# Performance work log

Hardware: AMD Instinct MI355X
Metric: run time of the kernel (lower is better)

## Reference

```python
import jax, jax.numpy as jnp
import numpy as np

B, N, M, D, OUT, K = 8, 32, 64, 128, 128, 3
EPS = 1e-5


def batchnorm(x, g, b):
    # training-mode BatchNorm2d over NCHW (stats over B,H,W per channel, biased var)
    mean = x.mean((0, 2, 3), keepdims=True)
    var = ((x - mean) ** 2).mean((0, 2, 3), keepdims=True)
    return g[None, :, None, None] * (x - mean) * jax.lax.rsqrt(var + EPS) + b[None, :, None, None]


def mycorr(x):
    # Pearson correlation between nodes along feature dim: x (B,M,N,D) -> (B,M,N,N)
    xc = x - x.mean(-1, keepdims=True)
    num = jnp.einsum('bmid,bmjd->bmij', xc, xc)
    nrm = jnp.sqrt((xc * xc).sum(-1))
    return num / (nrm[:, :, :, None] * nrm[:, :, None, :] + 1e-8)


def attention(x, W_fc1, W_fc2):
    # x: (B,M,N,D). AdaptiveAvgPool2d((None,1)) over the concat [Wh_i, pos*Wh_j]
    # equals 0.5*(mean_d Wh_i + mean_d(pos*Wh_j)); pos=1 where Wh_i==Wh_j else 2.
    adj = mycorr(x)
    mean_i = x.mean(-1)                       # (B,M,N)
    xi = x[:, :, :, None, :]                  # (B,M,N,1,D)
    xj = x[:, :, None, :, :]                  # (B,M,1,N,D)
    alt_mean = jnp.where(xi == xj, xj, 2.0 * xj).mean(-1)  # (B,M,N,N)
    e = 0.5 * (mean_i[:, :, :, None] + alt_mean)            # (B,M,N,N)
    ef = e.reshape(e.shape[0], e.shape[1], -1)              # (B,M,N*N) pair channels
    h = jax.nn.relu(jnp.einsum('rp,bmp->bmr', W_fc1, ef))
    e2 = jax.nn.sigmoid(jnp.einsum('pr,bmr->bmp', W_fc2, h)).reshape(e.shape)
    att = jax.nn.softmax(jnp.where(adj > 0, e2, jnp.float32(-1e12)), axis=-1)
    return jnp.einsum('bmij,bmjd->bmid', att, x)


def setup_inputs() -> dict:
    key = jax.random.key(0)
    ks = jax.random.split(key, 8)
    P, r, s = N * N, (N * N) // 2, 0.05
    return {
        'x': jax.random.normal(ks[0], (B, N, M, D), jnp.float32),
        'W_sc': jax.random.normal(ks[1], (OUT, M), jnp.float32) * s,
        'g_sc': jnp.ones(OUT, jnp.float32), 'b_sc': jnp.zeros(OUT, jnp.float32),
        'W_l1': jax.random.normal(ks[2], (M, M), jnp.float32) * s,
        'g1': jnp.ones(M, jnp.float32), 'b1': jnp.zeros(M, jnp.float32),
        'W_fc1': jax.random.normal(ks[3], (r, P), jnp.float32) * s,
        'W_fc2': jax.random.normal(ks[4], (P, r), jnp.float32) * s,
        'g2': jnp.ones(M, jnp.float32), 'b2': jnp.zeros(M, jnp.float32),
        'W_dw': jax.random.normal(ks[5], (N, 1, K, K), jnp.float32) * s,
        'g3': jnp.ones(N, jnp.float32), 'b3': jnp.zeros(N, jnp.float32),
        'W_l3': jax.random.normal(ks[6], (OUT, M), jnp.float32) * s,
    }


def reference(x, W_sc, g_sc, b_sc, W_l1, g1, b1, W_fc1, W_fc2, g2, b2, W_dw, g3, b3, W_l3):
    xm = jnp.transpose(x, (0, 2, 1, 3))  # (B,M,N,D)
    # shortcut: 1x1 conv over head channel + BN (stride=1 path)
    shortcut = batchnorm(jnp.einsum('om,bmnd->bond', W_sc, xm), g_sc, b_sc)
    # layer_1: 1x1 conv, BN, global node attention, BN, ReLU
    out = batchnorm(jnp.einsum('cm,bmnd->bcnd', W_l1, xm), g1, b1)
    out = attention(out, W_fc1, W_fc2)
    out = jax.nn.relu(batchnorm(out, g2, b2))
    # layer_2: depthwise KxK conv over (head, dim) per node, BN, ReLU
    out = jnp.transpose(out, (0, 2, 1, 3))  # (B,N,M,D)
    pad = K // 2
    out = jax.lax.conv_general_dilated(out, W_dw, (1, 1), ((pad, pad), (pad, pad)),
                                       feature_group_count=N,
                                       dimension_numbers=('NCHW', 'OIHW', 'NCHW'))
    out = jax.nn.relu(batchnorm(out, g3, b3))
    # layer_3: 1x1 conv to out_channels heads + residual
    out = jnp.transpose(out, (0, 2, 1, 3))  # (B,M,N,D)
    out = jnp.einsum('om,bmnd->bond', W_l3, out) + shortcut
    return jnp.transpose(out, (0, 2, 1, 3))  # (B,N,OUT,D)
```

## Files before the change

### kernel.cpp

```cpp
#include <hip/hip_runtime.h>
#include <math.h>

#define EPS 1e-5f


__device__ __forceinline__ void fma4(float4& a, float s, const float4& v) {
    a.x += s * v.x; a.y += s * v.y; a.z += s * v.z; a.w += s * v.w;
}

__global__ __launch_bounds__(256) void k0_prep(
    const float* __restrict__ Wsc, const float* __restrict__ Wl1,
    const float* __restrict__ Wl3, float* __restrict__ Wt,
    float* __restrict__ Wt3, float* __restrict__ stats)
{
    int idx = blockIdx.x * 256 + threadIdx.x;
    if (idx < 12288) {
        int m = idx / 192, cc = idx % 192;
        Wt[idx] = (cc < 128) ? Wsc[(size_t)cc * 64 + m]
                             : Wl1[(size_t)(cc - 128) * 64 + m];
    } else if (idx < 20480) {
        int k = idx - 12288;
        int m = k >> 7, o = k & 127;
        Wt3[k] = Wl3[(size_t)o * 64 + m];
    } else if (idx < 21504) {
        stats[idx - 20480] = 0.f;
    }
}

__global__ __launch_bounds__(256, 3) void k1_matmul_stats(
    const float* __restrict__ x, const float* __restrict__ Wt,
    const float* __restrict__ Wfc1, float* __restrict__ t_sc,
    float* __restrict__ t_l1, float* __restrict__ C1,
    float* __restrict__ stats)
{
    int g  = blockIdx.x;
    int bn = blockIdx.y;
    __shared__ __align__(16) float s_x[64 * 144];
    __shared__ __align__(16) float s_w[64 * 64];
    int t = threadIdx.x;

    if (g == 3) {
#pragma unroll
        for (int rr = 0; rr < 2; rr++) {
            int r = bn * 2 + rr;
            *(float4*)(s_x + t * 4) =
                *(const float4*)(Wfc1 + (size_t)r * 1024 + t * 4);
            __syncthreads();
            if (t < 32) {
                float rs = 0.f, cs = 0.f;
#pragma unroll
                for (int j = 0; j < 32; j++) {
                    rs += s_x[t * 32 + j];
                    cs += s_x[j * 32 + t];
                }
                C1[r * 32 + t] = (rs + 2.f * cs - s_x[t * 33]) * (1.0f / 256.0f);
            }
            __syncthreads();
        }
        return;
    }

    int b = bn >> 5, n = bn & 31;
    const float4* xg = (const float4*)(x + (size_t)bn * 8192);
    for (int i = t; i < 2048; i += 256) {
        int row = i >> 5, j = i & 31;
        *(float4*)(s_x + row * 144 + j * 4 + ((j >> 3) << 2)) = xg[i];
    }
    for (int i = t; i < 1024; i += 256) {
        int m = i >> 4, ch = (i & 15) * 4;
        *(float4*)(s_w + i * 4) =
            *(const float4*)(Wt + (size_t)m * 192 + g * 64 + ch);
    }
    __syncthreads();

    int wv = t >> 6, lane = t & 63;
    int dl = lane & 15, g4 = lane >> 4;
    int d0 = dl * 8;
    int c0 = wv * 16 + g4 * 4;
    int xoff = d0 + ((dl >> 2) << 2);

    float4 acc[4][2];
#pragma unroll
    for (int i = 0; i < 4; i++) { acc[i][0] = make_float4(0,0,0,0); acc[i][1] = make_float4(0,0,0,0); }

#pragma unroll 4
    for (int m = 0; m < 64; m += 2) {
        const float* xr = s_x + m * 144 + xoff;
        float4 x00 = *(const float4*)(xr);
        float4 x01 = *(const float4*)(xr + 4);
        float4 x10 = *(const float4*)(xr + 144);
        float4 x11 = *(const float4*)(xr + 148);
        float4 w0 = *(const float4*)(s_w + m * 64 + c0);
        float4 w1 = *(const float4*)(s_w + (m + 1) * 64 + c0);
        fma4(acc[0][0], w0.x, x00); fma4(acc[0][1], w0.x, x01);
        fma4(acc[1][0], w0.y, x00); fma4(acc[1][1], w0.y, x01);
        fma4(acc[2][0], w0.z, x00); fma4(acc[2][1], w0.z, x01);
        fma4(acc[3][0], w0.w, x00); fma4(acc[3][1], w0.w, x01);
        fma4(acc[0][0], w1.x, x10); fma4(acc[0][1], w1.x, x11);
        fma4(acc[1][0], w1.y, x10); fma4(acc[1][1], w1.y, x11);
        fma4(acc[2][0], w1.z, x10); fma4(acc[2][1], w1.z, x11);
        fma4(acc[3][0], w1.w, x10); fma4(acc[3][1], w1.w, x11);
    }

#pragma unroll
    for (int i = 0; i < 4; i++) {
        int cc = g * 64 + c0 + i;
        float4 v0 = acc[i][0], v1 = acc[i][1];
        float* dst;
        if (cc < 128) dst = t_sc + (((size_t)bn * 128 + cc)) * 128 + d0;
        else          dst = t_l1 + (((size_t)(b * 64 + (cc - 128))) * 32 + n) * 128 + d0;
        *(float4*)dst = v0;
        *(float4*)(dst + 4) = v1;
        float s = v0.x + v0.y + v0.z + v0.w + v1.x + v1.y + v1.z + v1.w;
        float q = v0.x*v0.x + v0.y*v0.y + v0.z*v0.z + v0.w*v0.w
                + v1.x*v1.x + v1.y*v1.y + v1.z*v1.z + v1.w*v1.w;
#pragma unroll
        for (int off = 8; off > 0; off >>= 1) {
            s += __shfl_down(s, off, 16);
            q += __shfl_down(q, off, 16);
        }
        if (dl == 0) {
            if (cc < 128) {
                atomicAdd(&stats[cc], s);
                atomicAdd(&stats[cc + 128], q);
            } else {
                atomicAdd(&stats[256 + (cc - 128)], s);
                atomicAdd(&stats[320 + (cc - 128)], q);
            }
        }
    }
}

__device__ __forceinline__ int yb(int r) { return r * 132 + ((r >> 2) << 3); }

__global__ __launch_bounds__(256) void k2_attn_prep(
    const float* __restrict__ t_l1, const float* __restrict__ g1,
    const float* __restrict__ b1, const float* __restrict__ stats,
    const float* __restrict__ Wfc1, const float* __restrict__ C1,
    float* __restrict__ y_g, float* __restrict__ H,
    unsigned int* __restrict__ maskbits)
{
    int bm = blockIdx.x;
    int t  = threadIdx.x;
    __shared__ __align__(16) float y_s[4288];
    __shared__ float S_s[32];
    __shared__ unsigned int m_s[32];
    __shared__ int anom_cnt;
    __shared__ int anom_p[64];
    __shared__ float anom_v[64];
    int m = bm & 63;
    float mean = stats[256 + m] * (1.0f / 32768.0f);
    float var  = stats[320 + m] * (1.0f / 32768.0f) - mean * mean;
    float a = g1[m] * rsqrtf(var + EPS);
    float c = b1[m] - a * mean;

    if (t == 0) anom_cnt = 0;
    if (t < 32) m_s[t] = 0u;
    const float4* src = (const float4*)(t_l1 + (size_t)bm * 4096);
    for (int i = t; i < 1024; i += 256) {
        float4 v = src[i];
        v.x = a * v.x + c; v.y = a * v.y + c; v.z = a * v.z + c; v.w = a * v.w + c;
        int row = i >> 5, col = (i & 31) * 4;
        *(float4*)(y_s + yb(row) + col) = v;
    }
    __syncthreads();

    {
        int r = t >> 3, j = t & 7;
        float s = 0.f;
        const float* yr = y_s + yb(r) + j * 16;
#pragma unroll
        for (int dd = 0; dd < 16; dd++) s += yr[dd];
#pragma unroll
        for (int off = 4; off > 0; off >>= 1) s += __shfl_down(s, off, 8);
        if (j == 0) S_s[r] = s;
    }
    __syncthreads();

    int i = t >> 3, j0 = (t & 7) * 4;
    float dot[4] = {0.f, 0.f, 0.f, 0.f};
    float eqs[4] = {0.f, 0.f, 0.f, 0.f};
    const float* yi = y_s + yb(i);
    const float* yj[4] = { y_s + yb(j0), y_s + yb(j0 + 1),
                           y_s + yb(j0 + 2), y_s + yb(j0 + 3) };
    for (int dq = 0; dq < 32; dq++) {
        float4 a4 = *(const float4*)(yi + dq * 4);
#pragma unroll
        for (int q = 0; q < 4; q++) {
            float4 b4 = *(const float4*)(yj[q] + dq * 4);
            dot[q] += a4.x * b4.x + a4.y * b4.y + a4.z * b4.z + a4.w * b4.w;
            eqs[q] += (a4.x == b4.x ? b4.x : 0.f) + (a4.y == b4.y ? b4.y : 0.f)
                    + (a4.z == b4.z ? b4.z : 0.f) + (a4.w == b4.w ? b4.w : 0.f);
        }
    }
    float Si = S_s[i];
    unsigned int bits = 0u;
#pragma unroll
    for (int q = 0; q < 4; q++) {
        int j = j0 + q;
        float Sj = S_s[j];
        float num = dot[q] - Si * Sj * (1.0f / 128.0f);
        if (num > 0.f) bits |= (1u << j);
        if (j != i && eqs[q] != 0.f) {
            int idx = atomicAdd(&anom_cnt, 1);
            if (idx < 64) {
                anom_p[idx] = i * 32 + j;
                anom_v[idx] = eqs[q] * (1.0f / 256.0f);
            }
        }
    }
    atomicOr(&m_s[i], bits);
    __syncthreads();
    if (t < 32) maskbits[bm * 32 + t] = m_s[t];

    int cnt = anom_cnt; if (cnt > 64) cnt = 64;
#pragma unroll
    for (int rr = 0; rr < 2; rr++) {
        int r = t * 2 + rr;
        const float4* c1r = (const float4*)(C1 + r * 32);
        float acc = 0.f;
#pragma unroll
        for (int kk = 0; kk < 8; kk++) {
            float4 cv = c1r[kk];
            acc += cv.x * S_s[kk * 4 + 0] + cv.y * S_s[kk * 4 + 1]
                 + cv.z * S_s[kk * 4 + 2] + cv.w * S_s[kk * 4 + 3];
        }
        for (int a2 = 0; a2 < cnt; a2++)
            acc -= Wfc1[(size_t)r * 1024 + anom_p[a2]] * anom_v[a2];
        H[(size_t)bm * 512 + r] = fmaxf(acc, 0.f);
    }

    float4* yd = (float4*)(y_g + (size_t)bm * 4096);
    for (int idx = t; idx < 1024; idx += 256) {
        int row = idx >> 5, col = (idx & 31) * 4;
        yd[idx] = *(const float4*)(y_s + yb(row) + col);
    }
}

template<int KDIM, int MODE>
__global__ __launch_bounds__(256) void k3_gemm(
    const float* __restrict__ A, const float* __restrict__ Bm,
    float* __restrict__ C, int NC)
{
    __shared__ __align__(16) float lds[4 * 2304];
    int t = threadIdx.x;
    int w = t >> 6, l = t & 63;
    int ct = blockIdx.x, rt = blockIdx.y;
    int row0 = rt * 32, col0 = ct * 32;
    float* As = lds + w * 2304;
    float* Bs = As + 1152;
    int rg = l >> 3;
    int cg = l & 7;
    int kq = (l & 7) * 4;
    constexpr int SLABS = KDIM / 128;

    float4 acc[4];
#pragma unroll
    for (int ii = 0; ii < 4; ii++) acc[ii] = make_float4(0,0,0,0);

    float4 av[4], bv[4], av2[4], bv2[4];
    int k0 = w * 32;
#pragma unroll
    for (int rr = 0; rr < 4; rr++) {
        int r = rg + rr * 8;
        av[rr] = *(const float4*)(A  + (size_t)(row0 + r) * KDIM + k0 + kq);
        bv[rr] = *(const float4*)(Bm + (size_t)(col0 + r) * KDIM + k0 + kq);
    }

    for (int s = 0; s < SLABS; s++) {
#pragma unroll
        for (int rr = 0; rr < 4; rr++) {
            int r = rg + rr * 8;
            As[(kq + 0) * 36 + r] = av[rr].x; As[(kq + 1) * 36 + r] = av[rr].y;
            As[(kq + 2) * 36 + r] = av[rr].z; As[(kq + 3) * 36 + r] = av[rr].w;
            Bs[(kq + 0) * 36 + r] = bv[rr].x; Bs[(kq + 1) * 36 + r] = bv[rr].y;
            Bs[(kq + 2) * 36 + r] = bv[rr].z; Bs[(kq + 3) * 36 + r] = bv[rr].w;
        }
        if (s + 1 < SLABS) {
            int kn = (4 * (s + 1) + w) * 32;
#pragma unroll
            for (int rr = 0; rr < 4; rr++) {
                int r = rg + rr * 8;
                av2[rr] = *(const float4*)(A  + (size_t)(row0 + r) * KDIM + kn + kq);
                bv2[rr] = *(const float4*)(Bm + (size_t)(col0 + r) * KDIM + kn + kq);
            }
        }
#pragma unroll
        for (int k = 0; k < 32; k++) {
            float4 a = *(const float4*)(As + k * 36 + rg * 4);
            float4 b = *(const float4*)(Bs + k * 36 + cg * 4);
            fma4(acc[0], a.x, b);
            fma4(acc[1], a.y, b);
            fma4(acc[2], a.z, b);
            fma4(acc[3], a.w, b);
        }
#pragma unroll
        for (int rr = 0; rr < 4; rr++) { av[rr] = av2[rr]; bv[rr] = bv2[rr]; }
    }

    __syncthreads();
    float* red = lds;
#pragma unroll
    for (int ii = 0; ii < 4; ii++)
        *(float4*)(red + w * 1024 + (rg * 4 + ii) * 32 + cg * 4) = acc[ii];
    __syncthreads();

    int r = t >> 3, c4 = (t & 7) * 4;
    float4 s0 = *(const float4*)(red + r * 32 + c4);
    float4 s1 = *(const float4*)(red + 1024 + r * 32 + c4);
    float4 s2 = *(const float4*)(red + 2048 + r * 32 + c4);
    float4 s3 = *(const float4*)(red + 3072 + r * 32 + c4);
    float4 v;
    v.x = s0.x + s1.x + s2.x + s3.x;
    v.y = s0.y + s1.y + s2.y + s3.y;
    v.z = s0.z + s1.z + s2.z + s3.z;
    v.w = s0.w + s1.w + s2.w + s3.w;
    if (MODE == 0) {
        v.x = fmaxf(v.x, 0.f); v.y = fmaxf(v.y, 0.f);
        v.z = fmaxf(v.z, 0.f); v.w = fmaxf(v.w, 0.f);
    } else {
        v.x = 1.0f / (1.0f + expf(-v.x)); v.y = 1.0f / (1.0f + expf(-v.y));
        v.z = 1.0f / (1.0f + expf(-v.z)); v.w = 1.0f / (1.0f + expf(-v.w));
    }
    *(float4*)(C + (size_t)(row0 + r) * NC + col0 + c4) = v;
}

__global__ __launch_bounds__(256) void k4_attn_apply(
    const float* __restrict__ E2, const unsigned int* __restrict__ maskbits,
    const float* __restrict__ y_g, float* __restrict__ att_out,
    float* __restrict__ stats)
{
    int bm = blockIdx.x;
    int t  = threadIdx.x;
    __shared__ __align__(16) float att_s[32 * 33];
    __shared__ __align__(16) float y_sh[32 * 128];
    __shared__ float redS[4], redQ[4];

    const float4* ysrc = (const float4*)(y_g + (size_t)bm * 4096);
    float4* yds = (float4*)y_sh;
    for (int i = t; i < 1024; i += 256) yds[i] = ysrc[i];

    {
        int r = t >> 3, j0 = (t & 7) * 4;
        unsigned int mk = maskbits[bm * 32 + r];
        float4 e4 = *(const float4*)(E2 + (size_t)bm * 1024 + r * 32 + j0);
        float v0 = ((mk >> (j0 + 0)) & 1u) ? e4.x : -1e12f;
        float v1 = ((mk >> (j0 + 1)) & 1u) ? e4.y : -1e12f;
        float v2 = ((mk >> (j0 + 2)) & 1u) ? e4.z : -1e12f;
        float v3 = ((mk >> (j0 + 3)) & 1u) ? e4.w : -1e12f;
        float mx = fmaxf(fmaxf(v0, v1), fmaxf(v2, v3));
#pragma unroll
        for (int off = 1; off < 8; off <<= 1) mx = fmaxf(mx, __shfl_xor(mx, off, 8));
        float e0 = __expf(v0 - mx), e1 = __expf(v1 - mx);
        float e2 = __expf(v2 - mx), e3 = __expf(v3 - mx);
        float s = e0 + e1 + e2 + e3;
#pragma unroll
        for (int off = 1; off < 8; off <<= 1) s += __shfl_xor(s, off, 8);
        float inv = 1.0f / s;
        att_s[r * 33 + j0 + 0] = e0 * inv;
        att_s[r * 33 + j0 + 1] = e1 * inv;
        att_s[r * 33 + j0 + 2] = e2 * inv;
        att_s[r * 33 + j0 + 3] = e3 * inv;
    }
    __syncthreads();

    int tx = t & 31, ty = t >> 5;
    int dq = tx * 4;
    int i0 = ty * 4;
    float4 acc0 = make_float4(0,0,0,0), acc1 = make_float4(0,0,0,0);
    float4 acc2 = make_float4(0,0,0,0), acc3 = make_float4(0,0,0,0);
    for (int j = 0; j < 32; j++) {
        float4 yv = *(const float4*)(y_sh + j * 128 + dq);
        float w0 = att_s[(i0 + 0) * 33 + j];
        float w1 = att_s[(i0 + 1) * 33 + j];
        float w2 = att_s[(i0 + 2) * 33 + j];
        float w3 = att_s[(i0 + 3) * 33 + j];
        fma4(acc0, w0, yv);
        fma4(acc1, w1, yv);
        fma4(acc2, w2, yv);
        fma4(acc3, w3, yv);
    }
    float ssum = 0.f, sq = 0.f;
    float4 accs[4] = {acc0, acc1, acc2, acc3};
#pragma unroll
    for (int ii = 0; ii < 4; ii++) {
        float4 acc = accs[ii];
        *(float4*)(att_out + (size_t)bm * 4096 + (i0 + ii) * 128 + dq) = acc;
        ssum += acc.x + acc.y + acc.z + acc.w;
        sq   += acc.x * acc.x + acc.y * acc.y + acc.z * acc.z + acc.w * acc.w;
    }
#pragma unroll
    for (int off = 32; off > 0; off >>= 1) {
        ssum += __shfl_down(ssum, off, 64);
        sq   += __shfl_down(sq, off, 64);
    }
    int wave = t >> 6, lane = t & 63;
    if (lane == 0) { redS[wave] = ssum; redQ[wave] = sq; }
    __syncthreads();
    if (t == 0) {
        float S = redS[0] + redS[1] + redS[2] + redS[3];
        float Q = redQ[0] + redQ[1] + redQ[2] + redQ[3];
        int m = bm & 63;
        atomicAdd(&stats[384 + m], S);
        atomicAdd(&stats[448 + m], Q);
    }
}

__global__ __launch_bounds__(256) void k5_conv(
    const float* __restrict__ att_out, const float* __restrict__ Wdw,
    const float* __restrict__ g2, const float* __restrict__ b2,
    float* __restrict__ stats, float* __restrict__ v_g)
{
    int bn = blockIdx.x;
    int b = bn >> 5, n = bn & 31;
    int t = threadIdx.x;
    __shared__ __align__(16) float z_s[66 * 130];
    __shared__ float a2_s[64], c2_s[64];
    __shared__ float redS[4], redQ[4];

    if (t < 64) {
        float mean = stats[384 + t] * (1.0f / 32768.0f);
        float var  = stats[448 + t] * (1.0f / 32768.0f) - mean * mean;
        float a = g2[t] * rsqrtf(var + EPS);
        a2_s[t] = a; c2_s[t] = b2[t] - a * mean;
    }
    for (int i = t; i < 66 * 130; i += 256) z_s[i] = 0.f;
    __syncthreads();

    for (int i = t; i < 2048; i += 256) {
        int m = i >> 5, c4 = (i & 31) * 4;
        float4 vv = *(const float4*)(att_out + (((size_t)(b * 64 + m)) * 32 + n) * 128 + c4);
        float a = a2_s[m], c = c2_s[m];
        float* dst = z_s + (m + 1) * 130 + c4 + 1;
        dst[0] = fmaxf(a * vv.x + c, 0.f);
        dst[1] = fmaxf(a * vv.y + c, 0.f);
        dst[2] = fmaxf(a * vv.z + c, 0.f);
        dst[3] = fmaxf(a * vv.w + c, 0.f);
    }
    float w[9];
#pragma unroll
    for (int i = 0; i < 9; i++) w[i] = Wdw[n * 9 + i];
    __syncthreads();

    int tx = t & 31, ty = t >> 5;
    int d0 = tx * 4;
    float ssum = 0.f, sq = 0.f;
#pragma unroll
    for (int rr = 0; rr < 8; rr++) {
        int h = ty * 8 + rr;
        float o0 = 0.f, o1 = 0.f, o2 = 0.f, o3 = 0.f;
#pragma unroll
        for (int dh = 0; dh < 3; dh++) {
            const float* zr = z_s + (h + dh) * 130 + d0;
#pragma unroll
            for (int dw = 0; dw < 3; dw++) {
                float wv = w[dh * 3 + dw];
                o0 += wv * zr[dw + 0];
                o1 += wv * zr[dw + 1];
                o2 += wv * zr[dw + 2];
                o3 += wv * zr[dw + 3];
            }
        }
        *(float4*)(v_g + ((size_t)bn * 64 + h) * 128 + d0) = make_float4(o0, o1, o2, o3);
        ssum += o0 + o1 + o2 + o3;
        sq   += o0 * o0 + o1 * o1 + o2 * o2 + o3 * o3;
    }
#pragma unroll
    for (int off = 32; off > 0; off >>= 1) {
        ssum += __shfl_down(ssum, off, 64);
        sq   += __shfl_down(sq, off, 64);
    }
    int wave = t >> 6, lane = t & 63;
    if (lane == 0) { redS[wave] = ssum; redQ[wave] = sq; }
    __syncthreads();
    if (t == 0) {
        atomicAdd(&stats[512 + n], redS[0] + redS[1] + redS[2] + redS[3]);
        atomicAdd(&stats[544 + n], redQ[0] + redQ[1] + redQ[2] + redQ[3]);
    }
}

__global__ __launch_bounds__(256, 3) void k6_final(
    const float* __restrict__ v_g, const float* __restrict__ t_sc,
    const float* __restrict__ Wt3, const float* __restrict__ g3,
    const float* __restrict__ b3, const float* __restrict__ gsc,
    const float* __restrict__ bsc, const float* __restrict__ stats,
    float* __restrict__ outp)
{
    int oh = blockIdx.x;
    int bn = blockIdx.y;
    int b = bn >> 5, n = bn & 31;
    int t = threadIdx.x;
    __shared__ __align__(16) float z_s[64 * 144];
    __shared__ __align__(16) float s_w[64 * 64];

    float mean3 = stats[512 + n] * (1.0f / 65536.0f);
    float var3  = stats[544 + n] * (1.0f / 65536.0f) - mean3 * mean3;
    float a3 = g3[n] * rsqrtf(var3 + EPS);
    float c3 = b3[n] - a3 * mean3;

    const float4* vsrc = (const float4*)(v_g + (size_t)bn * 8192);
    for (int i = t; i < 2048; i += 256) {
        float4 vv = vsrc[i];
        float4 r;
        r.x = fmaxf(a3 * vv.x + c3, 0.f);
        r.y = fmaxf(a3 * vv.y + c3, 0.f);
        r.z = fmaxf(a3 * vv.z + c3, 0.f);
        r.w = fmaxf(a3 * vv.w + c3, 0.f);
        int row = i >> 5, j = i & 31;
        *(float4*)(z_s + row * 144 + j * 4 + ((j >> 3) << 2)) = r;
    }
    for (int i = t; i < 1024; i += 256) {
        int m = i >> 4, ch = (i & 15) * 4;
        *(float4*)(s_w + i * 4) =
            *(const float4*)(Wt3 + (size_t)m * 128 + oh * 64 + ch);
    }
    __syncthreads();

    int wv = t >> 6, lane = t & 63;
    int dl = lane & 15, g4 = lane >> 4;
    int d0 = dl * 8;
    int c0 = wv * 16 + g4 * 4;
    int xoff = d0 + ((dl >> 2) << 2);

    float4 acc[4][2];
#pragma unroll
    for (int i = 0; i < 4; i++) { acc[i][0] = make_float4(0,0,0,0); acc[i][1] = make_float4(0,0,0,0); }

#pragma unroll 4
    for (int m = 0; m < 64; m += 2) {
        const float* xr = z_s + m * 144 + xoff;
        float4 x00 = *(const float4*)(xr);
        float4 x01 = *(const float4*)(xr + 4);
        float4 x10 = *(const float4*)(xr + 144);
        float4 x11 = *(const float4*)(xr + 148);
        float4 w0 = *(const float4*)(s_w + m * 64 + c0);
        float4 w1 = *(const float4*)(s_w + (m + 1) * 64 + c0);
        fma4(acc[0][0], w0.x, x00); fma4(acc[0][1], w0.x, x01);
        fma4(acc[1][0], w0.y, x00); fma4(acc[1][1], w0.y, x01);
        fma4(acc[2][0], w0.z, x00); fma4(acc[2][1], w0.z, x01);
        fma4(acc[3][0], w0.w, x00); fma4(acc[3][1], w0.w, x01);
        fma4(acc[0][0], w1.x, x10); fma4(acc[0][1], w1.x, x11);
        fma4(acc[1][0], w1.y, x10); fma4(acc[1][1], w1.y, x11);
        fma4(acc[2][0], w1.z, x10); fma4(acc[2][1], w1.z, x11);
        fma4(acc[3][0], w1.w, x10); fma4(acc[3][1], w1.w, x11);
    }

#pragma unroll
    for (int i = 0; i < 4; i++) {
        int o = oh * 64 + c0 + i;
        float msc = stats[o] * (1.0f / 32768.0f);
        float vsc = stats[128 + o] * (1.0f / 32768.0f) - msc * msc;
        float asc = gsc[o] * rsqrtf(vsc + EPS);
        float csc = bsc[o] - asc * msc;
        const float* ts = t_sc + ((size_t)bn * 128 + o) * 128 + d0;
        float4 t0 = *(const float4*)(ts);
        float4 t1 = *(const float4*)(ts + 4);
        float4 o0 = acc[i][0], o1 = acc[i][1];
        o0.x += asc * t0.x + csc; o0.y += asc * t0.y + csc;
        o0.z += asc * t0.z + csc; o0.w += asc * t0.w + csc;
        o1.x += asc * t1.x + csc; o1.y += asc * t1.y + csc;
        o1.z += asc * t1.z + csc; o1.w += asc * t1.w + csc;
        float* dst = outp + (((size_t)(b * 32 + n)) * 128 + o) * 128 + d0;
        *(float4*)dst = o0;
        *(float4*)(dst + 4) = o1;
    }
}

extern "C" void kernel_launch(void* const* d_in, const int* in_sizes, int n_in,
                              void* d_out, int out_size, void* d_ws, size_t ws_size,
                              hipStream_t stream)
{
    const float* x    = (const float*)d_in[0];
    const float* Wsc  = (const float*)d_in[1];
    const float* gsc  = (const float*)d_in[2];
    const float* bsc  = (const float*)d_in[3];
    const float* Wl1  = (const float*)d_in[4];
    const float* g1   = (const float*)d_in[5];
    const float* b1   = (const float*)d_in[6];
    const float* Wfc1 = (const float*)d_in[7];
    const float* Wfc2 = (const float*)d_in[8];
    const float* g2   = (const float*)d_in[9];
    const float* b2   = (const float*)d_in[10];
    const float* Wdw  = (const float*)d_in[11];
    const float* g3   = (const float*)d_in[12];
    const float* b3   = (const float*)d_in[13];
    const float* Wl3  = (const float*)d_in[14];
    float* outp = (float*)d_out;

    float* ws = (float*)d_ws;
    float* stats = ws;
    float* t_sc  = ws + 1024;
    float* t_l1  = t_sc + 4194304;
    float* y_g   = t_l1 + 2097152;
    float* C1    = y_g + 2097152;
    float* H     = C1 + 16384;
    float* E2    = H + 262144;
    unsigned int* maskb = (unsigned int*)(E2 + 524288);
    float* Wt    = (float*)(maskb + 16384);
    float* Wt3   = Wt + 12288;

    k0_prep<<<84, 256, 0, stream>>>(Wsc, Wl1, Wl3, Wt, Wt3, stats);
    k1_matmul_stats<<<dim3(4, 256), 256, 0, stream>>>(x, Wt, Wfc1, t_sc, t_l1, C1, stats);
    k2_attn_prep<<<512, 256, 0, stream>>>(t_l1, g1, b1, stats, Wfc1, C1, y_g, H, maskb);
    k3_gemm<512, 1><<<dim3(32, 16), 256, 0, stream>>>(H, Wfc2, E2, 1024);
    k4_attn_apply<<<512, 256, 0, stream>>>(E2, maskb, y_g, t_l1, stats);
    k5_conv<<<256, 256, 0, stream>>>(t_l1, Wdw, g2, b2, stats, y_g);
    k6_final<<<dim3(2, 256), 256, 0, stream>>>(y_g, t_sc, Wt3, g3, b3, gsc, bsc, stats, outp);
}
```

Measured before the change: 196.1 us.

## Fuse pipeline stages into persistent megakernel with global grid barriers

Replaces the six stage kernels after prep with one persistent kernel of 512 blocks. The stages are separated by a software grid barrier built on atomics in workspace memory, and the Wfc1 row/column-sum precompute moves into the prep kernel. The aim is to remove per-launch overhead and tail gaps between the small stages. In exchange, every stage is tied to a fixed 512-block decomposition with two blocks per CU, and the barrier can deadlock if not all blocks are co-resident.

```diff
diff --git a/kernel.cpp b/kernel.cpp
--- a/kernel.cpp
+++ b/kernel.cpp
@@ -2,6 +2,7 @@
 #include <math.h>
 
 #define EPS 1e-5f
+#define NBLK 512
 
 
 __device__ __forceinline__ void fma4(float4& a, float s, const float4& v) {
@@ -10,559 +11,579 @@
 
 __global__ __launch_bounds__(256) void k0_prep(
     const float* __restrict__ Wsc, const float* __restrict__ Wl1,
-    const float* __restrict__ Wl3, float* __restrict__ Wt,
-    float* __restrict__ Wt3, float* __restrict__ stats)
+    const float* __restrict__ Wl3, const float* __restrict__ Wfc1,
+    float* __restrict__ Wt, float* __restrict__ Wt3,
+    float* __restrict__ stats, unsigned int* __restrict__ bar,
+    float* __restrict__ C1)
 {
-    int idx = blockIdx.x * 256 + threadIdx.x;
-    if (idx < 12288) {
-        int m = idx / 192, cc = idx % 192;
-        Wt[idx] = (cc < 128) ? Wsc[(size_t)cc * 64 + m]
-                             : Wl1[(size_t)(cc - 128) * 64 + m];
-    } else if (idx < 20480) {
-        int k = idx - 12288;
-        int m = k >> 7, o = k & 127;
-        Wt3[k] = Wl3[(size_t)o * 64 + m];
-    } else if (idx < 21504) {
-        stats[idx - 20480] = 0.f;
-    }
-}
-
-__global__ __launch_bounds__(256, 3) void k1_matmul_stats(
-    const float* __restrict__ x, const float* __restrict__ Wt,
-    const float* __restrict__ Wfc1, float* __restrict__ t_sc,
-    float* __restrict__ t_l1, float* __restrict__ C1,
-    float* __restrict__ stats)
-{
-    int g  = blockIdx.x;
-    int bn = blockIdx.y;
-    __shared__ __align__(16) float s_x[64 * 144];
-    __shared__ __align__(16) float s_w[64 * 64];
+    int bx = blockIdx.x;
     int t = threadIdx.x;
-
-    if (g == 3) {
+    if (bx < 84) {
+        int idx = bx * 256 + t;
+        if (idx < 12288) {
+            int m = idx / 192, cc = idx % 192;
+            Wt[idx] = (cc < 128) ? Wsc[(size_t)cc * 64 + m]
+                                 : Wl1[(size_t)(cc - 128) * 64 + m];
+        } else if (idx < 20480) {
+            int k = idx - 12288;
+            int m = k >> 7, o = k & 127;
+            Wt3[k] = Wl3[(size_t)o * 64 + m];
+        } else if (idx < 21504) {
+            stats[idx - 20480] = 0.f;
+        }
+        if (idx == 0) { bar[0] = 0u; bar[1] = 0u; }
+    } else {
+        __shared__ float s[1024];
 #pragma unroll
         for (int rr = 0; rr < 2; rr++) {
-            int r = bn * 2 + rr;
-            *(float4*)(s_x + t * 4) =
+            int r = (bx - 84) * 2 + rr;
+            *(float4*)(s + t * 4) =
                 *(const float4*)(Wfc1 + (size_t)r * 1024 + t * 4);
             __syncthreads();
             if (t < 32) {
                 float rs = 0.f, cs = 0.f;
 #pragma unroll
                 for (int j = 0; j < 32; j++) {
-                    rs += s_x[t * 32 + j];
-                    cs += s_x[j * 32 + t];
+                    rs += s[t * 32 + j];
+                    cs += s[j * 32 + t];
                 }
-                C1[r * 32 + t] = (rs + 2.f * cs - s_x[t * 33]) * (1.0f / 256.0f);
+                C1[r * 32 + t] = (rs + 2.f * cs - s[t * 33]) * (1.0f / 256.0f);
             }
             __syncthreads();
         }
-        return;
-    }
-
-    int b = bn >> 5, n = bn & 31;
-    const float4* xg = (const float4*)(x + (size_t)bn * 8192);
-    for (int i = t; i < 2048; i += 256) {
-        int row = i >> 5, j = i & 31;
-        *(float4*)(s_x + row * 144 + j * 4 + ((j >> 3) << 2)) = xg[i];
-    }
-    for (int i = t; i < 1024; i += 256) {
-        int m = i >> 4, ch = (i & 15) * 4;
-        *(float4*)(s_w + i * 4) =
-            *(const float4*)(Wt + (size_t)m * 192 + g * 64 + ch);
-    }
+    }
+}
+
+__device__ __forceinline__ void gsync(unsigned int* bar) {
     __syncthreads();
-
-    int wv = t >> 6, lane = t & 63;
-    int dl = lane & 15, g4 = lane >> 4;
-    int d0 = dl * 8;
-    int c0 = wv * 16 + g4 * 4;
-    int xoff = d0 + ((dl >> 2) << 2);
-
-    float4 acc[4][2];
-#pragma unroll
-    for (int i = 0; i < 4; i++) { acc[i][0] = make_float4(0,0,0,0); acc[i][1] = make_float4(0,0,0,0); }
-
+    if (threadIdx.x == 0) {
+        __threadfence();
+        unsigned int g = __hip_atomic_load(bar + 1, __ATOMIC_ACQUIRE,
+                                           __HIP_MEMORY_SCOPE_AGENT);
+        unsigned int a = __hip_atomic_fetch_add(bar, 1u, __ATOMIC_ACQ_REL,
+                                                __HIP_MEMORY_SCOPE_AGENT);
+        if (a == NBLK - 1u) {
+            __hip_atomic_store(bar, 0u, __ATOMIC_RELAXED,
+                               __HIP_MEMORY_SCOPE_AGENT);
+            __hip_atomic_fetch_add(bar + 1, 1u, __ATOMIC_ACQ_REL,
+                                   __HIP_MEMORY_SCOPE_AGENT);
+        } else {
+            while (__hip_atomic_load(bar + 1, __ATOMIC_ACQUIRE,
+                                     __HIP_MEMORY_SCOPE_AGENT) == g)
+                __builtin_amdgcn_s_sleep(8);
+        }
+        __threadfence();
+    }
+    __syncthreads();
+}
+
+__device__ __forceinline__ int yb(int r) { return r * 132 + ((r >> 2) << 3); }
+
+__global__ __launch_bounds__(256, 2) void mega(
+    const float* __restrict__ x, const float* __restrict__ Wt,
+    const float* __restrict__ Wt3, const float* __restrict__ Wfc1,
+    const float* __restrict__ Wfc2,
+    const float* __restrict__ g1, const float* __restrict__ b1,
+    const float* __restrict__ g2, const float* __restrict__ b2,
+    const float* __restrict__ g3, const float* __restrict__ b3,
+    const float* __restrict__ gsc, const float* __restrict__ bsc,
+    const float* __restrict__ Wdw,
+    float* __restrict__ t_sc, float* __restrict__ t_l1,
+    float* __restrict__ y_g, float* __restrict__ C1,
+    float* __restrict__ H, float* __restrict__ E2,
+    unsigned int* __restrict__ maskb, float* __restrict__ stats,
+    unsigned int* __restrict__ bar, float* __restrict__ outp)
+{
+    __shared__ __align__(16) float smem[13312];
+    int bid = blockIdx.x;
+    int t = threadIdx.x;
+
+    {
+        float* s_x = smem;
+        float* s_w = smem + 9216;
+        for (int u = bid; u < 768; u += NBLK) {
+            __syncthreads();
+            int g = u >> 8, bn = u & 255;
+            int b = bn >> 5, n = bn & 31;
+            const float4* xg = (const float4*)(x + (size_t)bn * 8192);
+            for (int i = t; i < 2048; i += 256) {
+                int row = i >> 5, j = i & 31;
+                *(float4*)(s_x + row * 144 + j * 4 + ((j >> 3) << 2)) = xg[i];
+            }
+            for (int i = t; i < 1024; i += 256) {
+                int m = i >> 4, ch = (i & 15) * 4;
+                *(float4*)(s_w + i * 4) =
+                    *(const float4*)(Wt + (size_t)m * 192 + g * 64 + ch);
+            }
+            __syncthreads();
+
+            int wv = t >> 6, lane = t & 63;
+            int dl = lane & 15, g4 = lane >> 4;
+            int d0 = dl * 8;
+            int c0 = wv * 16 + g4 * 4;
+            int xoff = d0 + ((dl >> 2) << 2);
+
+            float4 acc[4][2];
+#pragma unroll
+            for (int i = 0; i < 4; i++) {
+                acc[i][0] = make_float4(0,0,0,0);
+                acc[i][1] = make_float4(0,0,0,0);
+            }
 #pragma unroll 4
-    for (int m = 0; m < 64; m += 2) {
-        const float* xr = s_x + m * 144 + xoff;
-        float4 x00 = *(const float4*)(xr);
-        float4 x01 = *(const float4*)(xr + 4);
-        float4 x10 = *(const float4*)(xr + 144);
-        float4 x11 = *(const float4*)(xr + 148);
-        float4 w0 = *(const float4*)(s_w + m * 64 + c0);
-        float4 w1 = *(const float4*)(s_w + (m + 1) * 64 + c0);
-        fma4(acc[0][0], w0.x, x00); fma4(acc[0][1], w0.x, x01);
-        fma4(acc[1][0], w0.y, x00); fma4(acc[1][1], w0.y, x01);
-        fma4(acc[2][0], w0.z, x00); fma4(acc[2][1], w0.z, x01);
-        fma4(acc[3][0], w0.w, x00); fma4(acc[3][1], w0.w, x01);
-        fma4(acc[0][0], w1.x, x10); fma4(acc[0][1], w1.x, x11);
-        fma4(acc[1][0], w1.y, x10); fma4(acc[1][1], w1.y, x11);
-        fma4(acc[2][0], w1.z, x10); fma4(acc[2][1], w1.z, x11);
-        fma4(acc[3][0], w1.w, x10); fma4(acc[3][1], w1.w, x11);
-    }
-
-#pragma unroll
-    for (int i = 0; i < 4; i++) {
-        int cc = g * 64 + c0 + i;
-        float4 v0 = acc[i][0], v1 = acc[i][1];
-        float* dst;
-        if (cc < 128) dst = t_sc + (((size_t)bn * 128 + cc)) * 128 + d0;
-        else          dst = t_l1 + (((size_t)(b * 64 + (cc - 128))) * 32 + n) * 128 + d0;
-        *(float4*)dst = v0;
-        *(float4*)(dst + 4) = v1;
-        float s = v0.x + v0.y + v0.z + v0.w + v1.x + v1.y + v1.z + v1.w;
-        float q = v0.x*v0.x + v0.y*v0.y + v0.z*v0.z + v0.w*v0.w
-                + v1.x*v1.x + v1.y*v1.y + v1.z*v1.z + v1.w*v1.w;
-#pragma unroll
-        for (int off = 8; off > 0; off >>= 1) {
-            s += __shfl_down(s, off, 16);
-            q += __shfl_down(q, off, 16);
-        }
-        if (dl == 0) {
-            if (cc < 128) {
-                atomicAdd(&stats[cc], s);
-                atomicAdd(&stats[cc + 128], q);
-            } else {
-                atomicAdd(&stats[256 + (cc - 128)], s);
-                atomicAdd(&stats[320 + (cc - 128)], q);
-            }
-        }
-    }
-}
-
-__device__ __forceinline__ int yb(int r) { return r * 132 + ((r >> 2) << 3); }
-
-__global__ __launch_bounds__(256) void k2_attn_prep(
-    const float* __restrict__ t_l1, const float* __restrict__ g1,
-    const float* __restrict__ b1, const float* __restrict__ stats,
-    const float* __restrict__ Wfc1, const float* __restrict__ C1,
-    float* __restrict__ y_g, float* __restrict__ H,
-    unsigned int* __restrict__ maskbits)
-{
-    int bm = blockIdx.x;
-    int t  = threadIdx.x;
-    __shared__ __align__(16) float y_s[4288];
-    __shared__ float S_s[32];
-    __shared__ unsigned int m_s[32];
-    __shared__ int anom_cnt;
-    __shared__ int anom_p[64];
-    __shared__ float anom_v[64];
-    int m = bm & 63;
-    float mean = stats[256 + m] * (1.0f / 32768.0f);
-    float var  = stats[320 + m] * (1.0f / 32768.0f) - mean * mean;
-    float a = g1[m] * rsqrtf(var + EPS);
-    float c = b1[m] - a * mean;
-
-    if (t == 0) anom_cnt = 0;
-    if (t < 32) m_s[t] = 0u;
-    const float4* src = (const float4*)(t_l1 + (size_t)bm * 4096);
-    for (int i = t; i < 1024; i += 256) {
-        float4 v = src[i];
-        v.x = a * v.x + c; v.y = a * v.y + c; v.z = a * v.z + c; v.w = a * v.w + c;
-        int row = i >> 5, col = (i & 31) * 4;
-        *(float4*)(y_s + yb(row) + col) = v;
-    }
-    __syncthreads();
+            for (int m = 0; m < 64; m += 2) {
+                const float* xr = s_x + m * 144 + xoff;
+                float4 x00 = *(const float4*)(xr);
+                float4 x01 = *(const float4*)(xr + 4);
+                float4 x10 = *(const float4*)(xr + 144);
+                float4 x11 = *(const float4*)(xr + 148);
+                float4 w0 = *(const float4*)(s_w + m * 64 + c0);
+                float4 w1 = *(const float4*)(s_w + (m + 1) * 64 + c0);
+                fma4(acc[0][0], w0.x, x00); fma4(acc[0][1], w0.x, x01);
+                fma4(acc[1][0], w0.y, x00); fma4(acc[1][1], w0.y, x01);
+                fma4(acc[2][0], w0.z, x00); fma4(acc[2][1], w0.z, x01);
+                fma4(acc[3][0], w0.w, x00); fma4(acc[3][1], w0.w, x01);
+                fma4(acc[0][0], w1.x, x10); fma4(acc[0][1], w1.x, x11);
+                fma4(acc[1][0], w1.y, x10); fma4(acc[1][1], w1.y, x11);
+                fma4(acc[2][0], w1.z, x10); fma4(acc[2][1], w1.z, x11);
+                fma4(acc[3][0], w1.w, x10); fma4(acc[3][1], w1.w, x11);
+            }
+#pragma unroll
+            for (int i = 0; i < 4; i++) {
+                int cc = g * 64 + c0 + i;
+                float4 v0 = acc[i][0], v1 = acc[i][1];
+                float* dst;
+                if (cc < 128) dst = t_sc + ((size_t)bn * 128 + cc) * 128 + d0;
+                else dst = t_l1 + (((size_t)(b * 64 + (cc - 128))) * 32 + n) * 128 + d0;
+                *(float4*)dst = v0;
+                *(float4*)(dst + 4) = v1;
+                float s = v0.x + v0.y + v0.z + v0.w + v1.x + v1.y + v1.z + v1.w;
+                float q = v0.x*v0.x + v0.y*v0.y + v0.z*v0.z + v0.w*v0.w
+                        + v1.x*v1.x + v1.y*v1.y + v1.z*v1.z + v1.w*v1.w;
+#pragma unroll
+                for (int off = 8; off > 0; off >>= 1) {
+                    s += __shfl_down(s, off, 16);
+                    q += __shfl_down(q, off, 16);
+                }
+                if (dl == 0) {
+                    if (cc < 128) {
+                        atomicAdd(&stats[cc], s);
+                        atomicAdd(&stats[cc + 128], q);
+                    } else {
+                        atomicAdd(&stats[256 + (cc - 128)], s);
+                        atomicAdd(&stats[320 + (cc - 128)], q);
+                    }
+                }
+            }
+        }
+    }
+    gsync(bar);
 
     {
-        int r = t >> 3, j = t & 7;
-        float s = 0.f;
-        const float* yr = y_s + yb(r) + j * 16;
-#pragma unroll
-        for (int dd = 0; dd < 16; dd++) s += yr[dd];
-#pragma unroll
-        for (int off = 4; off > 0; off >>= 1) s += __shfl_down(s, off, 8);
-        if (j == 0) S_s[r] = s;
-    }
-    __syncthreads();
-
-    int i = t >> 3, j0 = (t & 7) * 4;
-    float dot[4] = {0.f, 0.f, 0.f, 0.f};
-    float eqs[4] = {0.f, 0.f, 0.f, 0.f};
-    const float* yi = y_s + yb(i);
-    const float* yj[4] = { y_s + yb(j0), y_s + yb(j0 + 1),
-                           y_s + yb(j0 + 2), y_s + yb(j0 + 3) };
-    for (int dq = 0; dq < 32; dq++) {
-        float4 a4 = *(const float4*)(yi + dq * 4);
+        float* y_s = smem;
+        float* S_s = smem + 4288;
+        unsigned int* m_s = (unsigned int*)(smem + 4320);
+        int* anom_p = (int*)(smem + 4352);
+        float* anom_v = smem + 4416;
+        int* anom_cnt = (int*)(smem + 4480);
+
+        int bm = bid;
+        int m = bm & 63;
+        float mean = stats[256 + m] * (1.0f / 32768.0f);
+        float var  = stats[320 + m] * (1.0f / 32768.0f) - mean * mean;
+        float a = g1[m] * rsqrtf(var + EPS);
+        float c = b1[m] - a * mean;
+
+        if (t == 0) *anom_cnt = 0;
+        if (t < 32) m_s[t] = 0u;
+        const float4* src = (const float4*)(t_l1 + (size_t)bm * 4096);
+        for (int i = t; i < 1024; i += 256) {
+            float4 v = src[i];
+            v.x = a * v.x + c; v.y = a * v.y + c; v.z = a * v.z + c; v.w = a * v.w + c;
+            int row = i >> 5, col = (i & 31) * 4;
+            *(float4*)(y_s + yb(row) + col) = v;
+        }
+        __syncthreads();
+
+        {
+            int r = t >> 3, j = t & 7;
+            float s = 0.f;
+            const float* yr = y_s + yb(r) + j * 16;
+#pragma unroll
+            for (int dd = 0; dd < 16; dd++) s += yr[dd];
+#pragma unroll
+            for (int off = 4; off > 0; off >>= 1) s += __shfl_down(s, off, 8);
+            if (j == 0) S_s[r] = s;
+        }
+        __syncthreads();
+
+        int i = t >> 3, j0 = (t & 7) * 4;
+        float dot[4] = {0.f, 0.f, 0.f, 0.f};
+        float eqs[4] = {0.f, 0.f, 0.f, 0.f};
+        const float* yi = y_s + yb(i);
+        const float* yj[4] = { y_s + yb(j0), y_s + yb(j0 + 1),
+                               y_s + yb(j0 + 2), y_s + yb(j0 + 3) };
+        for (int dq = 0; dq < 32; dq++) {
+            float4 a4 = *(const float4*)(yi + dq * 4);
+#pragma unroll
+            for (int q = 0; q < 4; q++) {
+                float4 b4 = *(const float4*)(yj[q] + dq * 4);
+                dot[q] += a4.x * b4.x + a4.y * b4.y + a4.z * b4.z + a4.w * b4.w;
+                eqs[q] += (a4.x == b4.x ? b4.x : 0.f) + (a4.y == b4.y ? b4.y : 0.f)
+                        + (a4.z == b4.z ? b4.z : 0.f) + (a4.w == b4.w ? b4.w : 0.f);
+            }
+        }
+        float Si = S_s[i];
+        unsigned int bits = 0u;
 #pragma unroll
         for (int q = 0; q < 4; q++) {
-            float4 b4 = *(const float4*)(yj[q] + dq * 4);
-            dot[q] += a4.x * b4.x + a4.y * b4.y + a4.z * b4.z + a4.w * b4.w;
-            eqs[q] += (a4.x == b4.x ? b4.x : 0.f) + (a4.y == b4.y ? b4.y : 0.f)
-                    + (a4.z == b4.z ? b4.z : 0.f) + (a4.w == b4.w ? b4.w : 0.f);
-        }
-    }
-    float Si = S_s[i];
-    unsigned int bits = 0u;
-#pragma unroll
-    for (int q = 0; q < 4; q++) {
-        int j = j0 + q;
-        float Sj = S_s[j];
-        float num = dot[q] - Si * Sj * (1.0f / 128.0f);
-        if (num > 0.f) bits |= (1u << j);
-        if (j != i && eqs[q] != 0.f) {
-            int idx = atomicAdd(&anom_cnt, 1);
-            if (idx < 64) {
-                anom_p[idx] = i * 32 + j;
-                anom_v[idx] = eqs[q] * (1.0f / 256.0f);
-            }
-        }
-    }
-    atomicOr(&m_s[i], bits);
-    __syncthreads();
-    if (t < 32) maskbits[bm * 32 + t] = m_s[t];
-
-    int cnt = anom_cnt; if (cnt > 64) cnt = 64;
-#pragma unroll
-    for (int rr = 0; rr < 2; rr++) {
-        int r = t * 2 + rr;
-        const float4* c1r = (const float4*)(C1 + r * 32);
-        float acc = 0.f;
-#pragma unroll
-        for (int kk = 0; kk < 8; kk++) {
-            float4 cv = c1r[kk];
-            acc += cv.x * S_s[kk * 4 + 0] + cv.y * S_s[kk * 4 + 1]
-                 + cv.z * S_s[kk * 4 + 2] + cv.w * S_s[kk * 4 + 3];
-        }
-        for (int a2 = 0; a2 < cnt; a2++)
-            acc -= Wfc1[(size_t)r * 1024 + anom_p[a2]] * anom_v[a2];
-        H[(size_t)bm * 512 + r] = fmaxf(acc, 0.f);
-    }
-
-    float4* yd = (float4*)(y_g + (size_t)bm * 4096);
-    for (int idx = t; idx < 1024; idx += 256) {
-        int row = idx >> 5, col = (idx & 31) * 4;
-        yd[idx] = *(const float4*)(y_s + yb(row) + col);
-    }
-}
-
-template<int KDIM, int MODE>
-__global__ __launch_bounds__(256) void k3_gemm(
-    const float* __restrict__ A, const float* __restrict__ Bm,
-    float* __restrict__ C, int NC)
-{
-    __shared__ __align__(16) float lds[4 * 2304];
-    int t = threadIdx.x;
-    int w = t >> 6, l = t & 63;
-    int ct = blockIdx.x, rt = blockIdx.y;
-    int row0 = rt * 32, col0 = ct * 32;
-    float* As = lds + w * 2304;
-    float* Bs = As + 1152;
-    int rg = l >> 3;
-    int cg = l & 7;
-    int kq = (l & 7) * 4;
-    constexpr int SLABS = KDIM / 128;
-
-    float4 acc[4];
-#pragma unroll
-    for (int ii = 0; ii < 4; ii++) acc[ii] = make_float4(0,0,0,0);
-
-    float4 av[4], bv[4], av2[4], bv2[4];
-    int k0 = w * 32;
-#pragma unroll
-    for (int rr = 0; rr < 4; rr++) {
-        int r = rg + rr * 8;
-        av[rr] = *(const float4*)(A  + (size_t)(row0 + r) * KDIM + k0 + kq);
-        bv[rr] = *(const float4*)(Bm + (size_t)(col0 + r) * KDIM + k0 + kq);
-    }
-
-    for (int s = 0; s < SLABS; s++) {
+            int j = j0 + q;
+            float Sj = S_s[j];
+            float num = dot[q] - Si * Sj * (1.0f / 128.0f);
+            if (num > 0.f) bits |= (1u << j);
+            if (j != i && eqs[q] != 0.f) {
+                int idx = atomicAdd(anom_cnt, 1);
+                if (idx < 64) {
+                    anom_p[idx] = i * 32 + j;
+                    anom_v[idx] = eqs[q] * (1.0f / 256.0f);
+                }
+            }
+        }
+        atomicOr(&m_s[i], bits);
+        __syncthreads();
+        if (t < 32) maskb[bm * 32 + t] = m_s[t];
+
+        int cnt = *anom_cnt; if (cnt > 64) cnt = 64;
+#pragma unroll
+        for (int rr = 0; rr < 2; rr++) {
+            int r = t * 2 + rr;
+            const float4* c1r = (const float4*)(C1 + r * 32);
+            float acc = 0.f;
+#pragma unroll
+            for (int kk = 0; kk < 8; kk++) {
+                float4 cv = c1r[kk];
+                acc += cv.x * S_s[kk * 4 + 0] + cv.y * S_s[kk * 4 + 1]
+                     + cv.z * S_s[kk * 4 + 2] + cv.w * S_s[kk * 4 + 3];
+            }
+            for (int a2 = 0; a2 < cnt; a2++)
+                acc -= Wfc1[(size_t)r * 1024 + anom_p[a2]] * anom_v[a2];
+            H[(size_t)bm * 512 + r] = fmaxf(acc, 0.f);
+        }
+
+        float4* yd = (float4*)(y_g + (size_t)bm * 4096);
+        for (int idx = t; idx < 1024; idx += 256) {
+            int row = idx >> 5, col = (idx & 31) * 4;
+            yd[idx] = *(const float4*)(y_s + yb(row) + col);
+        }
+    }
+    gsync(bar);
+
+    {
+        float* lds = smem;
+        int w = t >> 6, l = t & 63;
+        int ct = bid & 31, rt = bid >> 5;
+        int row0 = rt * 32, col0 = ct * 32;
+        float* As = lds + w * 2304;
+        float* Bs = As + 1152;
+        int rg = l >> 3;
+        int cgi = l & 7;
+        int kq = (l & 7) * 4;
+        const int KDIM = 512;
+
+        float4 acc[4];
+#pragma unroll
+        for (int ii = 0; ii < 4; ii++) acc[ii] = make_float4(0,0,0,0);
+
+        float4 av[4], bv[4], av2[4], bv2[4];
+        int k0 = w * 32;
 #pragma unroll
         for (int rr = 0; rr < 4; rr++) {
             int r = rg + rr * 8;
-            As[(kq + 0) * 36 + r] = av[rr].x; As[(kq + 1) * 36 + r] = av[rr].y;
-            As[(kq + 2) * 36 + r] = av[rr].z; As[(kq + 3) * 36 + r] = av[rr].w;
-            Bs[(kq + 0) * 36 + r] = bv[rr].x; Bs[(kq + 1) * 36 + r] = bv[rr].y;
-            Bs[(kq + 2) * 36 + r] = bv[rr].z; Bs[(kq + 3) * 36 + r] = bv[rr].w;
-        }
-        if (s + 1 < SLABS) {
-            int kn = (4 * (s + 1) + w) * 32;
+            av[rr] = *(const float4*)(H    + (size_t)(row0 + r) * KDIM + k0 + kq);
+            bv[rr] = *(const float4*)(Wfc2 + (size_t)(col0 + r) * KDIM + k0 + kq);
+        }
+        for (int s = 0; s < 4; s++) {
 #pragma unroll
             for (int rr = 0; rr < 4; rr++) {
                 int r = rg + rr * 8;
-                av2[rr] = *(const float4*)(A  + (size_t)(row0 + r) * KDIM + kn + kq);
-                bv2[rr] = *(const float4*)(Bm + (size_t)(col0 + r) * KDIM + kn + kq);
-            }
-        }
-#pragma unroll
-        for (int k = 0; k < 32; k++) {
-            float4 a = *(const float4*)(As + k * 36 + rg * 4);
-            float4 b = *(const float4*)(Bs + k * 36 + cg * 4);
-            fma4(acc[0], a.x, b);
-            fma4(acc[1], a.y, b);
-            fma4(acc[2], a.z, b);
-            fma4(acc[3], a.w, b);
-        }
-#pragma unroll
-        for (int rr = 0; rr < 4; rr++) { av[rr] = av2[rr]; bv[rr] = bv2[rr]; }
-    }
-
-    __syncthreads();
-    float* red = lds;
-#pragma unroll
-    for (int ii = 0; ii < 4; ii++)
-        *(float4*)(red + w * 1024 + (rg * 4 + ii) * 32 + cg * 4) = acc[ii];
-    __syncthreads();
-
-    int r = t >> 3, c4 = (t & 7) * 4;
-    float4 s0 = *(const float4*)(red + r * 32 + c4);
-    float4 s1 = *(const float4*)(red + 1024 + r * 32 + c4);
-    float4 s2 = *(const float4*)(red + 2048 + r * 32 + c4);
-    float4 s3 = *(const float4*)(red + 3072 + r * 32 + c4);
-    float4 v;
-    v.x = s0.x + s1.x + s2.x + s3.x;
-    v.y = s0.y + s1.y + s2.y + s3.y;
-    v.z = s0.z + s1.z + s2.z + s3.z;
-    v.w = s0.w + s1.w + s2.w + s3.w;
-    if (MODE == 0) {
-        v.x = fmaxf(v.x, 0.f); v.y = fmaxf(v.y, 0.f);
-        v.z = fmaxf(v.z, 0.f); v.w = fmaxf(v.w, 0.f);
-    } else {
+                As[(kq + 0) * 36 + r] = av[rr].x; As[(kq + 1) * 36 + r] = av[rr].y;
+                As[(kq + 2) * 36 + r] = av[rr].z; As[(kq + 3) * 36 + r] = av[rr].w;
+                Bs[(kq + 0) * 36 + r] = bv[rr].x; Bs[(kq + 1) * 36 + r] = bv[rr].y;
+                Bs[(kq + 2) * 36 + r] = bv[rr].z; Bs[(kq + 3) * 36 + r] = bv[rr].w;
+            }
+            if (s + 1 < 4) {
+                int kn = (4 * (s + 1) + w) * 32;
+#pragma unroll
+                for (int rr = 0; rr < 4; rr++) {
+                    int r = rg + rr * 8;
+                    av2[rr] = *(const float4*)(H    + (size_t)(row0 + r) * KDIM + kn + kq);
+                    bv2[rr] = *(const float4*)(Wfc2 + (size_t)(col0 + r) * KDIM + kn + kq);
+                }
+            }
+#pragma unroll
+            for (int k = 0; k < 32; k++) {
+                float4 a = *(const float4*)(As + k * 36 + rg * 4);
+                float4 b = *(const float4*)(Bs + k * 36 + cgi * 4);
+                fma4(acc[0], a.x, b);
+                fma4(acc[1], a.y, b);
+                fma4(acc[2], a.z, b);
+                fma4(acc[3], a.w, b);
+            }
+#pragma unroll
+            for (int rr = 0; rr < 4; rr++) { av[rr] = av2[rr]; bv[rr] = bv2[rr]; }
+        }
+
+        __syncthreads();
+        float* red = lds;
+#pragma unroll
+        for (int ii = 0; ii < 4; ii++)
+            *(float4*)(red + w * 1024 + (rg * 4 + ii) * 32 + cgi * 4) = acc[ii];
+        __syncthreads();
+
+        int r = t >> 3, c4 = (t & 7) * 4;
+        float4 s0 = *(const float4*)(red + r * 32 + c4);
+        float4 s1 = *(const float4*)(red + 1024 + r * 32 + c4);
+        float4 s2 = *(const float4*)(red + 2048 + r * 32 + c4);
+        float4 s3 = *(const float4*)(red + 3072 + r * 32 + c4);
+        float4 v;
+        v.x = s0.x + s1.x + s2.x + s3.x;
+        v.y = s0.y + s1.y + s2.y + s3.y;
+        v.z = s0.z + s1.z + s2.z + s3.z;
+        v.w = s0.w + s1.w + s2.w + s3.w;
         v.x = 1.0f / (1.0f + expf(-v.x)); v.y = 1.0f / (1.0f + expf(-v.y));
         v.z = 1.0f / (1.0f + expf(-v.z)); v.w = 1.0f / (1.0f + expf(-v.w));
-    }
-    *(float4*)(C + (size_t)(row0 + r) * NC + col0 + c4) = v;
-}
-
-__global__ __launch_bounds__(256) void k4_attn_apply(
-    const float* __restrict__ E2, const unsigned int* __restrict__ maskbits,
-    const float* __restrict__ y_g, float* __restrict__ att_out,
-    float* __restrict__ stats)
-{
-    int bm = blockIdx.x;
-    int t  = threadIdx.x;
-    __shared__ __align__(16) float att_s[32 * 33];
-    __shared__ __align__(16) float y_sh[32 * 128];
-    __shared__ float redS[4], redQ[4];
-
-    const float4* ysrc = (const float4*)(y_g + (size_t)bm * 4096);
-    float4* yds = (float4*)y_sh;
-    for (int i = t; i < 1024; i += 256) yds[i] = ysrc[i];
+        *(float4*)(E2 + (size_t)(row0 + r) * 1024 + col0 + c4) = v;
+    }
+    gsync(bar);
 
     {
-        int r = t >> 3, j0 = (t & 7) * 4;
-        unsigned int mk = maskbits[bm * 32 + r];
-        float4 e4 = *(const float4*)(E2 + (size_t)bm * 1024 + r * 32 + j0);
-        float v0 = ((mk >> (j0 + 0)) & 1u) ? e4.x : -1e12f;
-        float v1 = ((mk >> (j0 + 1)) & 1u) ? e4.y : -1e12f;
-        float v2 = ((mk >> (j0 + 2)) & 1u) ? e4.z : -1e12f;
-        float v3 = ((mk >> (j0 + 3)) & 1u) ? e4.w : -1e12f;
-        float mx = fmaxf(fmaxf(v0, v1), fmaxf(v2, v3));
-#pragma unroll
-        for (int off = 1; off < 8; off <<= 1) mx = fmaxf(mx, __shfl_xor(mx, off, 8));
-        float e0 = __expf(v0 - mx), e1 = __expf(v1 - mx);
-        float e2 = __expf(v2 - mx), e3 = __expf(v3 - mx);
-        float s = e0 + e1 + e2 + e3;
-#pragma unroll
-        for (int off = 1; off < 8; off <<= 1) s += __shfl_xor(s, off, 8);
-        float inv = 1.0f / s;
-        att_s[r * 33 + j0 + 0] = e0 * inv;
-        att_s[r * 33 + j0 + 1] = e1 * inv;
-        att_s[r * 33 + j0 + 2] = e2 * inv;
-        att_s[r * 33 + j0 + 3] = e3 * inv;
-    }
-    __syncthreads();
-
-    int tx = t & 31, ty = t >> 5;
-    int dq = tx * 4;
-    int i0 = ty * 4;
-    float4 acc0 = make_float4(0,0,0,0), acc1 = make_float4(0,0,0,0);
-    float4 acc2 = make_float4(0,0,0,0), acc3 = make_float4(0,0,0,0);
-    for (int j = 0; j < 32; j++) {
-        float4 yv = *(const float4*)(y_sh + j * 128 + dq);
-        float w0 = att_s[(i0 + 0) * 33 + j];
-        float w1 = att_s[(i0 + 1) * 33 + j];
-        float w2 = att_s[(i0 + 2) * 33 + j];
-        float w3 = att_s[(i0 + 3) * 33 + j];
-        fma4(acc0, w0, yv);
-        fma4(acc1, w1, yv);
-        fma4(acc2, w2, yv);
-        fma4(acc3, w3, yv);
-    }
-    float ssum = 0.f, sq = 0.f;
-    float4 accs[4] = {acc0, acc1, acc2, acc3};
-#pragma unroll
-    for (int ii = 0; ii < 4; ii++) {
-        float4 acc = accs[ii];
-        *(float4*)(att_out + (size_t)bm * 4096 + (i0 + ii) * 128 + dq) = acc;
-        ssum += acc.x + acc.y + acc.z + acc.w;
-        sq   += acc.x * acc.x + acc.y * acc.y + acc.z * acc.z + acc.w * acc.w;
-    }
-#pragma unroll
-    for (int off = 32; off > 0; off >>= 1) {
-        ssum += __shfl_down(ssum, off, 64);
-        sq   += __shfl_down(sq, off, 64);
-    }
-    int wave = t >> 6, lane = t & 63;
-    if (lane == 0) { redS[wave] = ssum; redQ[wave] = sq; }
-    __syncthreads();
-    if (t == 0) {
-        float S = redS[0] + redS[1] + redS[2] + redS[3];
-        float Q = redQ[0] + redQ[1] + redQ[2] + redQ[3];
-        int m = bm & 63;
-        atomicAdd(&stats[384 + m], S);
-        atomicAdd(&stats[448 + m], Q);
-    }
-}
-
-__global__ __launch_bounds__(256) void k5_conv(
-    const float* __restrict__ att_out, const float* __restrict__ Wdw,
-    const float* __restrict__ g2, const float* __restrict__ b2,
-    float* __restrict__ stats, float* __restrict__ v_g)
-{
-    int bn = blockIdx.x;
-    int b = bn >> 5, n = bn & 31;
-    int t = threadIdx.x;
-    __shared__ __align__(16) float z_s[66 * 130];
-    __shared__ float a2_s[64], c2_s[64];
-    __shared__ float redS[4], redQ[4];
-
-    if (t < 64) {
-        float mean = stats[384 + t] * (1.0f / 32768.0f);
-        float var  = stats[448 + t] * (1.0f / 32768.0f) - mean * mean;
-        float a = g2[t] * rsqrtf(var + EPS);
-        a2_s[t] = a; c2_s[t] = b2[t] - a * mean;
-    }
-    for (int i = t; i < 66 * 130; i += 256) z_s[i] = 0.f;
-    __syncthreads();
-
-    for (int i = t; i < 2048; i += 256) {
-        int m = i >> 5, c4 = (i & 31) * 4;
-        float4 vv = *(const float4*)(att_out + (((size_t)(b * 64 + m)) * 32 + n) * 128 + c4);
-        float a = a2_s[m], c = c2_s[m];
-        float* dst = z_s + (m + 1) * 130 + c4 + 1;
-        dst[0] = fmaxf(a * vv.x + c, 0.f);
-        dst[1] = fmaxf(a * vv.y + c, 0.f);
-        dst[2] = fmaxf(a * vv.z + c, 0.f);
-        dst[3] = fmaxf(a * vv.w + c, 0.f);
-    }
-    float w[9];
-#pragma unroll
-    for (int i = 0; i < 9; i++) w[i] = Wdw[n * 9 + i];
-    __syncthreads();
-
-    int tx = t & 31, ty = t >> 5;
-    int d0 = tx * 4;
-    float ssum = 0.f, sq = 0.f;
-#pragma unroll
-    for (int rr = 0; rr < 8; rr++) {
-        int h = ty * 8 + rr;
-        float o0 = 0.f, o1 = 0.f, o2 = 0.f, o3 = 0.f;
-#pragma unroll
-        for (int dh = 0; dh < 3; dh++) {
-            const float* zr = z_s + (h + dh) * 130 + d0;
-#pragma unroll
-            for (int dw = 0; dw < 3; dw++) {
-                float wv = w[dh * 3 + dw];
-                o0 += wv * zr[dw + 0];
-                o1 += wv * zr[dw + 1];
-                o2 += wv * zr[dw + 2];
-                o3 += wv * zr[dw + 3];
-            }
-        }
-        *(float4*)(v_g + ((size_t)bn * 64 + h) * 128 + d0) = make_float4(o0, o1, o2, o3);
-        ssum += o0 + o1 + o2 + o3;
-        sq   += o0 * o0 + o1 * o1 + o2 * o2 + o3 * o3;
-    }
-#pragma unroll
-    for (int off = 32; off > 0; off >>= 1) {
-        ssum += __shfl_down(ssum, off, 64);
-        sq   += __shfl_down(sq, off, 64);
-    }
-    int wave = t >> 6, lane = t & 63;
-    if (lane == 0) { redS[wave] = ssum; redQ[wave] = sq; }
-    __syncthreads();
-    if (t == 0) {
-        atomicAdd(&stats[512 + n], redS[0] + redS[1] + redS[2] + redS[3]);
-        atomicAdd(&stats[544 + n], redQ[0] + redQ[1] + redQ[2] + redQ[3]);
-    }
-}
-
-__global__ __launch_bounds__(256, 3) void k6_final(
-    const float* __restrict__ v_g, const float* __restrict__ t_sc,
-    const float* __restrict__ Wt3, const float* __restrict__ g3,
-    const float* __restrict__ b3, const float* __restrict__ gsc,
-    const float* __restrict__ bsc, const float* __restrict__ stats,
-    float* __restrict__ outp)
-{
-    int oh = blockIdx.x;
-    int bn = blockIdx.y;
-    int b = bn >> 5, n = bn & 31;
-    int t = threadIdx.x;
-    __shared__ __align__(16) float z_s[64 * 144];
-    __shared__ __align__(16) float s_w[64 * 64];
-
-    float mean3 = stats[512 + n] * (1.0f / 65536.0f);
-    float var3  = stats[544 + n] * (1.0f / 65536.0f) - mean3 * mean3;
-    float a3 = g3[n] * rsqrtf(var3 + EPS);
-    float c3 = b3[n] - a3 * mean3;
-
-    const float4* vsrc = (const float4*)(v_g + (size_t)bn * 8192);
-    for (int i = t; i < 2048; i += 256) {
-        float4 vv = vsrc[i];
-        float4 r;
-        r.x = fmaxf(a3 * vv.x + c3, 0.f);
-        r.y = fmaxf(a3 * vv.y + c3, 0.f);
-        r.z = fmaxf(a3 * vv.z + c3, 0.f);
-        r.w = fmaxf(a3 * vv.w + c3, 0.f);
-        int row = i >> 5, j = i & 31;
-        *(float4*)(z_s + row * 144 + j * 4 + ((j >> 3) << 2)) = r;
-    }
-    for (int i = t; i < 1024; i += 256) {
-        int m = i >> 4, ch = (i & 15) * 4;
-        *(float4*)(s_w + i * 4) =
-            *(const float4*)(Wt3 + (size_t)m * 128 + oh * 64 + ch);
-    }
-    __syncthreads();
-
-    int wv = t >> 6, lane = t & 63;
-    int dl = lane & 15, g4 = lane >> 4;
-    int d0 = dl * 8;
-    int c0 = wv * 16 + g4 * 4;
-    int xoff = d0 + ((dl >> 2) << 2);
-
-    float4 acc[4][2];
-#pragma unroll
-    for (int i = 0; i < 4; i++) { acc[i][0] = make_float4(0,0,0,0); acc[i][1] = make_float4(0,0,0,0); }
-
+        float* att_s = smem;
+        float* y_sh = smem + 1056;
+        float* redS = smem + 5152;
+        float* redQ = smem + 5156;
+
+        int bm = bid;
+        const float4* ysrc = (const float4*)(y_g + (size_t)bm * 4096);
+        float4* yds = (float4*)y_sh;
+        for (int i = t; i < 1024; i += 256) yds[i] = ysrc[i];
+
+        {
+            int r = t >> 3, j0 = (t & 7) * 4;
+            unsigned int mk = maskb[bm * 32 + r];
+            float4 e4 = *(const float4*)(E2 + (size_t)bm * 1024 + r * 32 + j0);
+            float v0 = ((mk >> (j0 + 0)) & 1u) ? e4.x : -1e12f;
+            float v1 = ((mk >> (j0 + 1)) & 1u) ? e4.y : -1e12f;
+            float v2 = ((mk >> (j0 + 2)) & 1u) ? e4.z : -1e12f;
+            float v3 = ((mk >> (j0 + 3)) & 1u) ? e4.w : -1e12f;
+            float mx = fmaxf(fmaxf(v0, v1), fmaxf(v2, v3));
+#pragma unroll
+            for (int off = 1; off < 8; off <<= 1) mx = fmaxf(mx, __shfl_xor(mx, off, 8));
+            float e0 = __expf(v0 - mx), e1 = __expf(v1 - mx);
+            float e2 = __expf(v2 - mx), e3 = __expf(v3 - mx);
+            float s = e0 + e1 + e2 + e3;
+#pragma unroll
+            for (int off = 1; off < 8; off <<= 1) s += __shfl_xor(s, off, 8);
+            float inv = 1.0f / s;
+            att_s[r * 33 + j0 + 0] = e0 * inv;
+            att_s[r * 33 + j0 + 1] = e1 * inv;
+            att_s[r * 33 + j0 + 2] = e2 * inv;
+            att_s[r * 33 + j0 + 3] = e3 * inv;
+        }
+        __syncthreads();
+
+        int tx = t & 31, ty = t >> 5;
+        int dq = tx * 4;
+        int i0 = ty * 4;
+        float4 acc0 = make_float4(0,0,0,0), acc1 = make_float4(0,0,0,0);
+        float4 acc2 = make_float4(0,0,0,0), acc3 = make_float4(0,0,0,0);
+        for (int j = 0; j < 32; j++) {
+            float4 yv = *(const float4*)(y_sh + j * 128 + dq);
+            float w0 = att_s[(i0 + 0) * 33 + j];
+            float w1 = att_s[(i0 + 1) * 33 + j];
+            float w2 = att_s[(i0 + 2) * 33 + j];
+            float w3 = att_s[(i0 + 3) * 33 + j];
+            fma4(acc0, w0, yv);
+            fma4(acc1, w1, yv);
+            fma4(acc2, w2, yv);
+            fma4(acc3, w3, yv);
+        }
+        float ssum = 0.f, sq = 0.f;
+        float4 accs[4] = {acc0, acc1, acc2, acc3};
+#pragma unroll
+        for (int ii = 0; ii < 4; ii++) {
+            float4 acc = accs[ii];
+            *(float4*)(t_l1 + (size_t)bm * 4096 + (i0 + ii) * 128 + dq) = acc;
+            ssum += acc.x + acc.y + acc.z + acc.w;
+            sq   += acc.x * acc.x + acc.y * acc.y + acc.z * acc.z + acc.w * acc.w;
+        }
+#pragma unroll
+        for (int off = 32; off > 0; off >>= 1) {
+            ssum += __shfl_down(ssum, off, 64);
+            sq   += __shfl_down(sq, off, 64);
+        }
+        int wave = t >> 6, lane = t & 63;
+        if (lane == 0) { redS[wave] = ssum; redQ[wave] = sq; }
+        __syncthreads();
+        if (t == 0) {
+            float S = redS[0] + redS[1] + redS[2] + redS[3];
+            float Q = redQ[0] + redQ[1] + redQ[2] + redQ[3];
+            int m = bm & 63;
+            atomicAdd(&stats[384 + m], S);
+            atomicAdd(&stats[448 + m], Q);
+        }
+    }
+    gsync(bar);
+
+    if (bid < 256) {
+        float* z_s = smem;
+        float* a2_s = smem + 8580;
+        float* c2_s = smem + 8644;
+        float* redS = smem + 8708;
+        float* redQ = smem + 8712;
+
+        int bn = bid;
+        int b = bn >> 5, n = bn & 31;
+        if (t < 64) {
+            float mean = stats[384 + t] * (1.0f / 32768.0f);
+            float var  = stats[448 + t] * (1.0f / 32768.0f) - mean * mean;
+            float a = g2[t] * rsqrtf(var + EPS);
+            a2_s[t] = a; c2_s[t] = b2[t] - a * mean;
+        }
+        for (int i = t; i < 66 * 130; i += 256) z_s[i] = 0.f;
+        __syncthreads();
+
+        for (int i = t; i < 2048; i += 256) {
+            int m = i >> 5, c4 = (i & 31) * 4;
+            float4 vv = *(const float4*)(t_l1 + (((size_t)(b * 64 + m)) * 32 + n) * 128 + c4);
+            float a = a2_s[m], c = c2_s[m];
+            float* dst = z_s + (m + 1) * 130 + c4 + 1;
+            dst[0] = fmaxf(a * vv.x + c, 0.f);
+            dst[1] = fmaxf(a * vv.y + c, 0.f);
+            dst[2] = fmaxf(a * vv.z + c, 0.f);
+            dst[3] = fmaxf(a * vv.w + c, 0.f);
+        }
+        float w[9];
+#pragma unroll
+        for (int i = 0; i < 9; i++) w[i] = Wdw[n * 9 + i];
+        __syncthreads();
+
+        int tx = t & 31, ty = t >> 5;
+        int d0 = tx * 4;
+        float ssum = 0.f, sq = 0.f;
+#pragma unroll
+        for (int rr = 0; rr < 8; rr++) {
+            int h = ty * 8 + rr;
+            float o0 = 0.f, o1 = 0.f, o2 = 0.f, o3 = 0.f;
+#pragma unroll
+            for (int dh = 0; dh < 3; dh++) {
+                const float* zr = z_s + (h + dh) * 130 + d0;
+#pragma unroll
+                for (int dw = 0; dw < 3; dw++) {
+                    float wv = w[dh * 3 + dw];
+                    o0 += wv * zr[dw + 0];
+                    o1 += wv * zr[dw + 1];
+                    o2 += wv * zr[dw + 2];
+                    o3 += wv * zr[dw + 3];
+                }
+            }
+            *(float4*)(y_g + ((size_t)bn * 64 + h) * 128 + d0) = make_float4(o0, o1, o2, o3);
+            ssum += o0 + o1 + o2 + o3;
+            sq   += o0 * o0 + o1 * o1 + o2 * o2 + o3 * o3;
+        }
+#pragma unroll
+        for (int off = 32; off > 0; off >>= 1) {
+            ssum += __shfl_down(ssum, off, 64);
+            sq   += __shfl_down(sq, off, 64);
+        }
+        int wave = t >> 6, lane = t & 63;
+        if (lane == 0) { redS[wave] = ssum; redQ[wave] = sq; }
+        __syncthreads();
+        if (t == 0) {
+            atomicAdd(&stats[512 + n], redS[0] + redS[1] + redS[2] + redS[3]);
+            atomicAdd(&stats[544 + n], redQ[0] + redQ[1] + redQ[2] + redQ[3]);
+        }
+    }
+    gsync(bar);
+
+    {
+        float* z_s = smem;
+        float* s_w = smem + 9216;
+
+        int oh = bid >> 8, bn = bid & 255;
+        int b = bn >> 5, n = bn & 31;
+
+        float mean3 = stats[512 + n] * (1.0f / 65536.0f);
+        float var3  = stats[544 + n] * (1.0f / 65536.0f) - mean3 * mean3;
+        float a3 = g3[n] * rsqrtf(var3 + EPS);
+        float c3 = b3[n] - a3 * mean3;
+
+        const float4* vsrc = (const float4*)(y_g + (size_t)bn * 8192);
+        for (int i = t; i < 2048; i += 256) {
+            float4 vv = vsrc[i];
+            float4 r;
+            r.x = fmaxf(a3 * vv.x + c3, 0.f);
+            r.y = fmaxf(a3 * vv.y + c3, 0.f);
+            r.z = fmaxf(a3 * vv.z + c3, 0.f);
+            r.w = fmaxf(a3 * vv.w + c3, 0.f);
+            int row = i >> 5, j = i & 31;
+            *(float4*)(z_s + row * 144 + j * 4 + ((j >> 3) << 2)) = r;
+        }
+        for (int i = t; i < 1024; i += 256) {
+            int m = i >> 4, ch = (i & 15) * 4;
+            *(float4*)(s_w + i * 4) =
+                *(const float4*)(Wt3 + (size_t)m * 128 + oh * 64 + ch);
+        }
+        __syncthreads();
+
+        int wv = t >> 6, lane = t & 63;
+        int dl = lane & 15, g4 = lane >> 4;
+        int d0 = dl * 8;
+        int c0 = wv * 16 + g4 * 4;
+        int xoff = d0 + ((dl >> 2) << 2);
+
+        float4 acc[4][2];
+#pragma unroll
+        for (int i = 0; i < 4; i++) {
+            acc[i][0] = make_float4(0,0,0,0);
+            acc[i][1] = make_float4(0,0,0,0);
+        }
 #pragma unroll 4
-    for (int m = 0; m < 64; m += 2) {
-        const float* xr = z_s + m * 144 + xoff;
-        float4 x00 = *(const float4*)(xr);
-        float4 x01 = *(const float4*)(xr + 4);
-        float4 x10 = *(const float4*)(xr + 144);
-        float4 x11 = *(const float4*)(xr + 148);
-        float4 w0 = *(const float4*)(s_w + m * 64 + c0);
-        float4 w1 = *(const float4*)(s_w + (m + 1) * 64 + c0);
-        fma4(acc[0][0], w0.x, x00); fma4(acc[0][1], w0.x, x01);
-        fma4(acc[1][0], w0.y, x00); fma4(acc[1][1], w0.y, x01);
-        fma4(acc[2][0], w0.z, x00); fma4(acc[2][1], w0.z, x01);
-        fma4(acc[3][0], w0.w, x00); fma4(acc[3][1], w0.w, x01);
-        fma4(acc[0][0], w1.x, x10); fma4(acc[0][1], w1.x, x11);
-        fma4(acc[1][0], w1.y, x10); fma4(acc[1][1], w1.y, x11);
-        fma4(acc[2][0], w1.z, x10); fma4(acc[2][1], w1.z, x11);
-        fma4(acc[3][0], w1.w, x10); fma4(acc[3][1], w1.w, x11);
-    }
-
-#pragma unroll
-    for (int i = 0; i < 4; i++) {
-        int o = oh * 64 + c0 + i;
-        float msc = stats[o] * (1.0f / 32768.0f);
-        float vsc = stats[128 + o] * (1.0f / 32768.0f) - msc * msc;
-        float asc = gsc[o] * rsqrtf(vsc + EPS);
-        float csc = bsc[o] - asc * msc;
-        const float* ts = t_sc + ((size_t)bn * 128 + o) * 128 + d0;
-        float4 t0 = *(const float4*)(ts);
-        float4 t1 = *(const float4*)(ts + 4);
-        float4 o0 = acc[i][0], o1 = acc[i][1];
-        o0.x += asc * t0.x + csc; o0.y += asc * t0.y + csc;
-        o0.z += asc * t0.z + csc; o0.w += asc * t0.w + csc;
-        o1.x += asc * t1.x + csc; o1.y += asc * t1.y + csc;
-        o1.z += asc * t1.z + csc; o1.w += asc * t1.w + csc;
-        float* dst = outp + (((size_t)(b * 32 + n)) * 128 + o) * 128 + d0;
-        *(float4*)dst = o0;
-        *(float4*)(dst + 4) = o1;
+        for (int m = 0; m < 64; m += 2) {
+            const float* xr = z_s + m * 144 + xoff;
+            float4 x00 = *(const float4*)(xr);
+            float4 x01 = *(const float4*)(xr + 4);
+            float4 x10 = *(const float4*)(xr + 144);
+            float4 x11 = *(const float4*)(xr + 148);
+            float4 w0 = *(const float4*)(s_w + m * 64 + c0);
+            float4 w1 = *(const float4*)(s_w + (m + 1) * 64 + c0);
+            fma4(acc[0][0], w0.x, x00); fma4(acc[0][1], w0.x, x01);
+            fma4(acc[1][0], w0.y, x00); fma4(acc[1][1], w0.y, x01);
+            fma4(acc[2][0], w0.z, x00); fma4(acc[2][1], w0.z, x01);
+            fma4(acc[3][0], w0.w, x00); fma4(acc[3][1], w0.w, x01);
+            fma4(acc[0][0], w1.x, x10); fma4(acc[0][1], w1.x, x11);
+            fma4(acc[1][0], w1.y, x10); fma4(acc[1][1], w1.y, x11);
+            fma4(acc[2][0], w1.z, x10); fma4(acc[2][1], w1.z, x11);
+            fma4(acc[3][0], w1.w, x10); fma4(acc[3][1], w1.w, x11);
+        }
+
+#pragma unroll
+        for (int i = 0; i < 4; i++) {
+            int o = oh * 64 + c0 + i;
+            float msc = stats[o] * (1.0f / 32768.0f);
+            float vsc = stats[128 + o] * (1.0f / 32768.0f) - msc * msc;
+            float asc = gsc[o] * rsqrtf(vsc + EPS);
+            float csc = bsc[o] - asc * msc;
+            const float* ts = t_sc + ((size_t)bn * 128 + o) * 128 + d0;
+            float4 t0 = *(const float4*)(ts);
+            float4 t1 = *(const float4*)(ts + 4);
+            float4 o0 = acc[i][0], o1 = acc[i][1];
+            o0.x += asc * t0.x + csc; o0.y += asc * t0.y + csc;
+            o0.z += asc * t0.z + csc; o0.w += asc * t0.w + csc;
+            o1.x += asc * t1.x + csc; o1.y += asc * t1.y + csc;
+            o1.z += asc * t1.z + csc; o1.w += asc * t1.w + csc;
+            float* dst = outp + (((size_t)(b * 32 + n)) * 128 + o) * 128 + d0;
+            *(float4*)dst = o0;
+            *(float4*)(dst + 4) = o1;
+        }
     }
 }
 
@@ -598,12 +619,10 @@
     unsigned int* maskb = (unsigned int*)(E2 + 524288);
     float* Wt    = (float*)(maskb + 16384);
     float* Wt3   = Wt + 12288;
-
-    k0_prep<<<84, 256, 0, stream>>>(Wsc, Wl1, Wl3, Wt, Wt3, stats);
-    k1_matmul_stats<<<dim3(4, 256), 256, 0, stream>>>(x, Wt, Wfc1, t_sc, t_l1, C1, stats);
-    k2_attn_prep<<<512, 256, 0, stream>>>(t_l1, g1, b1, stats, Wfc1, C1, y_g, H, maskb);
-    k3_gemm<512, 1><<<dim3(32, 16), 256, 0, stream>>>(H, Wfc2, E2, 1024);
-    k4_attn_apply<<<512, 256, 0, stream>>>(E2, maskb, y_g, t_l1, stats);
-    k5_conv<<<256, 256, 0, stream>>>(t_l1, Wdw, g2, b2, stats, y_g);
-    k6_final<<<dim3(2, 256), 256, 0, stream>>>(y_g, t_sc, Wt3, g3, b3, gsc, bsc, stats, outp);
+    unsigned int* bar = (unsigned int*)(Wt3 + 8192);
+
+    k0_prep<<<212, 256, 0, stream>>>(Wsc, Wl1, Wl3, Wfc1, Wt, Wt3, stats, bar, C1);
+    mega<<<NBLK, 256, 0, stream>>>(
+        x, Wt, Wt3, Wfc1, Wfc2, g1, b1, g2, b2, g3, b3, gsc, bsc, Wdw,
+        t_sc, t_l1, y_g, C1, H, E2, maskb, stats, bar, outp);
 }
```

New measurement: 600.8 us. 206% more time.
